# Kernel optimization log

Hardware: AMD Instinct MI355X
Metric: run time of the kernel (lower is better)

The kernel has to match this reference:

```python
import jax, jax.numpy as jnp
import numpy as np

N = 50000
E = 1600000
INDIM, HIDIM, OUTDIM = 256, 128, 64


def setup_inputs() -> dict:
    key = jax.random.key(0)
    ks = jax.random.split(key, 4)
    x = jax.random.normal(ks[0], (N, INDIM), dtype=jnp.float32)
    edge_index = jax.random.randint(ks[1], (2, E), 0, N, dtype=jnp.int32)
    W1 = jax.random.normal(ks[2], (INDIM, HIDIM), dtype=jnp.float32) / np.float32(np.sqrt(INDIM))
    b1 = jnp.zeros((HIDIM,), dtype=jnp.float32)
    W2 = jax.random.normal(ks[3], (HIDIM, OUTDIM), dtype=jnp.float32) / np.float32(np.sqrt(HIDIM))
    b2 = jnp.zeros((OUTDIM,), dtype=jnp.float32)
    return {"x": x, "edge_index": edge_index, "W1": W1, "b1": b1, "W2": W2, "b2": b2}


def _gcn_conv(x, row, col, norm, W, b):
    # PyG GCNConv: transform first, then normalized scatter-add aggregation, then bias
    h = x @ W                              # [N, out]
    msg = h[row] * norm[:, None]           # gather source features, scale by edge norm
    out = jax.ops.segment_sum(msg, col, num_segments=x.shape[0])  # scatter-add to dst
    return out + b


def reference(x, edge_index, W1, b1, W2, b2):
    n = x.shape[0]
    # add self loops (PyG default add_self_loops=True)
    loops = jnp.arange(n, dtype=edge_index.dtype)
    row = jnp.concatenate([edge_index[0], loops])  # source nodes
    col = jnp.concatenate([edge_index[1], loops])  # destination nodes
    # symmetric normalization: deg^{-1/2}[row] * deg^{-1/2}[col], deg over dst incl. self loops
    deg = jax.ops.segment_sum(jnp.ones_like(col, dtype=x.dtype), col, num_segments=n)
    dinv = jnp.where(deg > 0, jax.lax.rsqrt(jnp.maximum(deg, 1.0)), 0.0)
    norm = dinv[row] * dinv[col]
    h = jax.nn.relu(_gcn_conv(x, row, col, norm, W1, b1))
    return _gcn_conv(h, row, col, norm, W2, b2)
```

## Files before the change

### kernel.cpp

```cpp
#include <hip/hip_runtime.h>

#define NN 50000
#define NE 1600000
#define INDIM 256
#define HIDIM 128
#define OUTDIM 64

#define NRANGE 128
#define RSPAN 400
#define ACAP 16384
#define NBBLK 1563
#define NDEG 256

typedef unsigned int uint;
typedef unsigned long long ull;
typedef unsigned short ushort;
typedef __attribute__((ext_vector_type(8))) short bf16x8;
typedef __attribute__((ext_vector_type(4))) float f32x4;

__device__ __forceinline__ ushort f2bf(float f) {
    uint u = __float_as_uint(f);
    uint r = (u + 0x7FFFu + ((u >> 16) & 1u)) >> 16;
    return (ushort)r;
}
__device__ __forceinline__ uint pk2(float a, float b) {
    return (uint)f2bf(a) | ((uint)f2bf(b) << 16);
}
__device__ __forceinline__ float bf_lo(uint u) { return __uint_as_float(u << 16); }
__device__ __forceinline__ float bf_hi(uint u) { return __uint_as_float(u & 0xFFFF0000u); }

#define ACC8(u) do { \
    a0 += bf_lo((u).x); a1 += bf_hi((u).x); \
    a2 += bf_lo((u).y); a3 += bf_hi((u).y); \
    a4 += bf_lo((u).z); a5 += bf_hi((u).z); \
    a6 += bf_lo((u).w); a7 += bf_hi((u).w); \
} while (0)


__global__ void k_wt(const float* __restrict__ W1, const float* __restrict__ W2,
                     ushort* __restrict__ W1T, ushort* __restrict__ W2T) {
    int idx = blockIdx.x * 256 + threadIdx.x;
    if (idx < INDIM * HIDIM) {
        int k = idx / HIDIM, nn = idx % HIDIM;
        W1T[nn * INDIM + k] = f2bf(W1[idx]);
    } else {
        int j = idx - INDIM * HIDIM;
        if (j < HIDIM * OUTDIM) {
            int k = j / OUTDIM, nn = j % OUTDIM;
            W2T[nn * HIDIM + k] = f2bf(W2[j]);
        }
    }
}


__global__ void k_bcnt(const int* __restrict__ col, int* __restrict__ bcnt,
                       int* __restrict__ dhist) {
    __shared__ int bins[NRANGE];
    int tid = threadIdx.x;
    if (blockIdx.x == 0) dhist[tid] = 0;
    if (tid < NRANGE) bins[tid] = 0;
    __syncthreads();
    int base = blockIdx.x * 1024 + tid;
#pragma unroll
    for (int k = 0; k < 4; k++) {
        int i = base + k * 256;
        if (i < NE) atomicAdd(&bins[col[i] / RSPAN], 1);
    }
    __syncthreads();
    if (tid < NRANGE) bcnt[tid * NBBLK + blockIdx.x] = bins[tid];
}


__global__ void k_bscan(const int* __restrict__ bcnt, int* __restrict__ bbase,
                        int* __restrict__ rcur) {
    __shared__ int wsum[16];
    __shared__ int woff[16];
    int r = blockIdx.x;
    const int* src = bcnt + r * NBBLK;
    int* dst = bbase + r * NBBLK;
    int tid = threadIdx.x, lane = tid & 63, wid = tid >> 6;
    int seg = tid * 2;
    int l0 = (seg < NBBLK) ? src[seg] : 0;
    int l1 = (seg + 1 < NBBLK) ? src[seg + 1] : 0;
    int sum = l0 + l1;
    int incl = sum;
#pragma unroll
    for (int off = 1; off < 64; off <<= 1) {
        int t = __shfl_up(incl, off);
        if (lane >= off) incl += t;
    }
    if (lane == 63) wsum[wid] = incl;
    __syncthreads();
    if (wid == 0 && lane < 16) {
        int wv = wsum[lane];
        int wincl = wv;
#pragma unroll
        for (int off = 1; off < 16; off <<= 1) {
            int t = __shfl_up(wincl, off);
            if (lane >= off) wincl += t;
        }
        woff[lane] = wincl - wv;
    }
    __syncthreads();
    int run = incl - sum + woff[wid];
    if (seg < NBBLK) dst[seg] = run;
    if (seg + 1 < NBBLK) dst[seg + 1] = run + l0;
    if (tid == 1023) rcur[r] = run + sum;
}


__global__ void k_bscat(const int* __restrict__ row, const int* __restrict__ col,
                        const int* __restrict__ bbase, uint* __restrict__ staged) {
    __shared__ int cur[NRANGE];
    int tid = threadIdx.x;
    if (tid < NRANGE) cur[tid] = bbase[tid * NBBLK + blockIdx.x];
    __syncthreads();
    int base = blockIdx.x * 1024 + tid;
#pragma unroll
    for (int k = 0; k < 4; k++) {
        int i = base + k * 256;
        if (i < NE) {
            int d = col[i], s = row[i];
            int r = d / RSPAN;
            int off = atomicAdd(&cur[r], 1);
            staged[(size_t)r * ACAP + off] = ((uint)s << 10) | (uint)(d - r * RSPAN);
        }
    }
}


__global__ void k_sort(const uint* __restrict__ staged, const int* __restrict__ rcur,
                       int* __restrict__ row_ptr, float* __restrict__ dinv,
                       ushort* __restrict__ ssrc, int* __restrict__ dhist) {
    __shared__ int bins[RSPAN];
    __shared__ int wsum[16];
    __shared__ int woff[16];
    __shared__ int dh[NDEG];
    int r = blockIdx.x;
    int tid = threadIdx.x, lane = tid & 63, wid = tid >> 6;
    int lo = r * RSPAN;
    int count = rcur[r];
    int base = 0;
    for (int rr = 0; rr < r; rr++) base += rcur[rr];
    const uint* st = staged + (size_t)r * ACAP;

    if (tid < RSPAN) bins[tid] = 0;
    if (tid < NDEG) dh[tid] = 0;
    __syncthreads();

    for (int i = tid; i < count; i += 1024)
        atomicAdd(&bins[st[i] & 1023u], 1);
    __syncthreads();

    int v = (tid < RSPAN) ? bins[tid] : 0;
    int incl = v;
#pragma unroll
    for (int off = 1; off < 64; off <<= 1) {
        int t = __shfl_up(incl, off);
        if (lane >= off) incl += t;
    }
    if (lane == 63) wsum[wid] = incl;
    __syncthreads();
    if (wid == 0 && lane < 16) {
        int wv = wsum[lane];
        int wincl = wv;
#pragma unroll
        for (int off = 1; off < 16; off <<= 1) {
            int t = __shfl_up(wincl, off);
            if (lane >= off) wincl += t;
        }
        woff[lane] = wincl - wv;
    }
    __syncthreads();
    int excl = incl - v + woff[wid];
    int idx = lo + tid;
    if (tid < RSPAN && idx <= NN) {
        if (idx < NN) {
            row_ptr[idx] = base + excl;
            dinv[idx] = rsqrtf((float)(v + 1));
            atomicAdd(&dh[min(v, NDEG - 1)], 1);
        } else {
            row_ptr[NN] = base + excl;
        }
    }
    __syncthreads();
    if (tid < RSPAN) bins[tid] = base + excl;
    __syncthreads();
    if (tid < NDEG && dh[tid]) atomicAdd(&dhist[tid], dh[tid]);

    for (int i = tid; i < count; i += 1024) {
        uint rec = st[i];
        int pos = atomicAdd(&bins[rec & 1023u], 1);
        ssrc[pos] = (ushort)(rec >> 10);
    }
}


__global__ void k_dscan(const int* __restrict__ dhist, int* __restrict__ dcur) {
    int lane = threadIdx.x;
    int b = lane * 4;
    int v0 = dhist[b], v1 = dhist[b + 1], v2 = dhist[b + 2], v3 = dhist[b + 3];
    int s = v0 + v1 + v2 + v3;
    int incl = s;
#pragma unroll
    for (int off = 1; off < 64; off <<= 1) {
        int t = __shfl_up(incl, off);
        if (lane >= off) incl += t;
    }
    int excl = incl - s;
    dcur[b] = excl;
    dcur[b + 1] = excl + v0;
    dcur[b + 2] = excl + v0 + v1;
    dcur[b + 3] = excl + v0 + v1 + v2;
}


__global__ void k_dscat(const int* __restrict__ row_ptr, int* __restrict__ dcur,
                        int* __restrict__ perm) {
    __shared__ int h[NDEG];
    __shared__ int boff[NDEG];
    int tid = threadIdx.x;
    int d = blockIdx.x * 256 + tid;
    h[tid] = 0;
    __syncthreads();
    int bin = 0, myoff = 0;
    if (d < NN) {
        int deg = row_ptr[d + 1] - row_ptr[d];
        bin = min(deg, NDEG - 1);
        myoff = atomicAdd(&h[bin], 1);
    }
    __syncthreads();
    if (h[tid]) boff[tid] = atomicAdd(&dcur[tid], h[tid]);
    __syncthreads();
    if (d < NN) perm[boff[bin] + myoff] = d;
}


__global__ void k_gemm1(const float* __restrict__ A, const ushort* __restrict__ W1T,
                        const float* __restrict__ dinv, ushort* __restrict__ g1s, int n) {
    __shared__ ushort As[64 * 40];
    __shared__ ushort Bs[128 * 40];
    int tid = threadIdx.x;
    int w = tid >> 6, lane = tid & 63;
    int ln = lane & 15, quad = lane >> 4;
    int row0 = blockIdx.x * 64;
    int n0 = w * 32;

    f32x4 acc[4][2];
#pragma unroll
    for (int m = 0; m < 4; m++)
#pragma unroll
        for (int t = 0; t < 2; t++) acc[m][t] = (f32x4){0.f, 0.f, 0.f, 0.f};

    int ar = tid >> 2;
    int ac = (tid & 3) * 8;

    for (int k0 = 0; k0 < INDIM; k0 += 32) {
        {
            int gr = row0 + ar;
            uint4 u = make_uint4(0, 0, 0, 0);
            if (gr < n) {
                const float* p = A + (size_t)gr * INDIM + k0 + ac;
                float4 v0 = *(const float4*)p;
                float4 v1 = *(const float4*)(p + 4);
                u.x = pk2(v0.x, v0.y); u.y = pk2(v0.z, v0.w);
                u.z = pk2(v1.x, v1.y); u.w = pk2(v1.z, v1.w);
            }
            *(uint4*)(As + ar * 40 + ac) = u;
        }
#pragma unroll
        for (int it = 0; it < 2; it++) {
            int idx = tid + it * 256;
            int bn = idx >> 2, bc = (idx & 3) * 8;
            uint4 u = *(const uint4*)(W1T + (size_t)bn * INDIM + k0 + bc);
            *(uint4*)(Bs + bn * 40 + bc) = u;
        }
        __syncthreads();

        bf16x8 af[4], bf[2];
#pragma unroll
        for (int m = 0; m < 4; m++)
            af[m] = *(const bf16x8*)(As + (m * 16 + ln) * 40 + quad * 8);
#pragma unroll
        for (int t = 0; t < 2; t++)
            bf[t] = *(const bf16x8*)(Bs + (n0 + t * 16 + ln) * 40 + quad * 8);
#pragma unroll
        for (int m = 0; m < 4; m++)
#pragma unroll
            for (int t = 0; t < 2; t++)
                acc[m][t] = __builtin_amdgcn_mfma_f32_16x16x32_bf16(af[m], bf[t], acc[m][t], 0, 0, 0);
        __syncthreads();
    }

    int slice = w >> 1;
    int fbase = (w & 1) * 32;
#pragma unroll
    for (int m = 0; m < 4; m++) {
#pragma unroll
        for (int r = 0; r < 4; r++) {
            int gr = row0 + m * 16 + quad * 4 + r;
            if (gr < n) {
                float dv = dinv[gr];
#pragma unroll
                for (int t = 0; t < 2; t++) {
                    int cj = t * 16 + ln;
                    g1s[((size_t)slice * NN + gr) * 64 + fbase + cj] = f2bf(acc[m][t][r] * dv);
                }
            }
        }
    }
}


__global__ void k_agg1(const ushort* __restrict__ g1s, const float* __restrict__ dinv,
                       const int* __restrict__ row_ptr, const ushort* __restrict__ ssrc,
                       const int* __restrict__ perm, const float* __restrict__ b1,
                       ushort* __restrict__ hrb) {
    int slice = blockIdx.x & 1;
    int dbase = (blockIdx.x >> 1) * 32;
    int wid = threadIdx.x >> 6, lane = threadIdx.x & 63;
    int grp = lane >> 3, fl = lane & 7;
    int di = dbase + wid * 8 + grp;
    if (di >= NN) return;
    int d = perm[di];
    const ushort* gs = g1s + (size_t)slice * NN * 64 + fl * 8;
    float a0 = 0.f, a1 = 0.f, a2 = 0.f, a3 = 0.f;
    float a4 = 0.f, a5 = 0.f, a6 = 0.f, a7 = 0.f;
    int e0 = row_ptr[d], e1 = row_ptr[d + 1];
    if (e1 > e0) {
        int last = e1 - 1;
        int sB0 = ssrc[min(e0 + 0, last)];
        int sB1 = ssrc[min(e0 + 1, last)];
        int sB2 = ssrc[min(e0 + 2, last)];
        int sB3 = ssrc[min(e0 + 3, last)];
        uint4 uA0 = *(const uint4*)(gs + (size_t)sB0 * 64);
        uint4 uA1 = *(const uint4*)(gs + (size_t)sB1 * 64);
        uint4 uA2 = *(const uint4*)(gs + (size_t)sB2 * 64);
        uint4 uA3 = *(const uint4*)(gs + (size_t)sB3 * 64);
        sB0 = ssrc[min(e0 + 4, last)];
        sB1 = ssrc[min(e0 + 5, last)];
        sB2 = ssrc[min(e0 + 6, last)];
        sB3 = ssrc[min(e0 + 7, last)];
        for (int eb = e0; eb < e1; eb += 4) {
            int p0 = ssrc[min(eb + 8, last)];
            int p1 = ssrc[min(eb + 9, last)];
            int p2 = ssrc[min(eb + 10, last)];
            int p3 = ssrc[min(eb + 11, last)];
            uint4 v0 = *(const uint4*)(gs + (size_t)sB0 * 64);
            uint4 v1 = *(const uint4*)(gs + (size_t)sB1 * 64);
            uint4 v2 = *(const uint4*)(gs + (size_t)sB2 * 64);
            uint4 v3 = *(const uint4*)(gs + (size_t)sB3 * 64);
            uint4 z = make_uint4(0u, 0u, 0u, 0u);
            if (eb + 1 >= e1) uA1 = z;
            if (eb + 2 >= e1) uA2 = z;
            if (eb + 3 >= e1) uA3 = z;
            ACC8(uA0); ACC8(uA1); ACC8(uA2); ACC8(uA3);
            uA0 = v0; uA1 = v1; uA2 = v2; uA3 = v3;
            sB0 = p0; sB1 = p1; sB2 = p2; sB3 = p3;
        }
    }
    uint4 ud = *(const uint4*)(gs + (size_t)d * 64);
    ACC8(ud);
    float dv = dinv[d];
    const float* bp = b1 + slice * 64 + fl * 8;
    float4 bb0 = *(const float4*)bp;
    float4 bb1 = *(const float4*)(bp + 4);
    uint4 o;
    o.x = pk2(fmaxf(a0 * dv + bb0.x, 0.f), fmaxf(a1 * dv + bb0.y, 0.f));
    o.y = pk2(fmaxf(a2 * dv + bb0.z, 0.f), fmaxf(a3 * dv + bb0.w, 0.f));
    o.z = pk2(fmaxf(a4 * dv + bb1.x, 0.f), fmaxf(a5 * dv + bb1.y, 0.f));
    o.w = pk2(fmaxf(a6 * dv + bb1.z, 0.f), fmaxf(a7 * dv + bb1.w, 0.f));
    *(uint4*)(hrb + ((size_t)slice * NN + d) * 64 + fl * 8) = o;
}


__global__ void k_gemm2(const ushort* __restrict__ hrb, const ushort* __restrict__ W2T,
                        const float* __restrict__ dinv, ushort* __restrict__ g2s, int n) {
    __shared__ ushort As[64 * 40];
    __shared__ ushort Bs[64 * 40];
    int tid = threadIdx.x;
    int w = tid >> 6, lane = tid & 63;
    int ln = lane & 15, quad = lane >> 4;
    int row0 = blockIdx.x * 64;
    int n0 = w * 16;

    f32x4 acc[4];
#pragma unroll
    for (int m = 0; m < 4; m++) acc[m] = (f32x4){0.f, 0.f, 0.f, 0.f};

    int ar = tid >> 2;
    int ac = (tid & 3) * 8;

    for (int k0 = 0; k0 < HIDIM; k0 += 32) {
        {
            int gr = row0 + ar;
            uint4 u = make_uint4(0, 0, 0, 0);
            if (gr < n) u = *(const uint4*)(hrb + ((size_t)(k0 >> 6) * NN + gr) * 64 + (k0 & 63) + ac);
            *(uint4*)(As + ar * 40 + ac) = u;
        }
        {
            int bn = tid >> 2, bc = (tid & 3) * 8;
            uint4 u = *(const uint4*)(W2T + (size_t)bn * HIDIM + k0 + bc);
            *(uint4*)(Bs + bn * 40 + bc) = u;
        }
        __syncthreads();

        bf16x8 bf = *(const bf16x8*)(Bs + (n0 + ln) * 40 + quad * 8);
#pragma unroll
        for (int m = 0; m < 4; m++) {
            bf16x8 af = *(const bf16x8*)(As + (m * 16 + ln) * 40 + quad * 8);
            acc[m] = __builtin_amdgcn_mfma_f32_16x16x32_bf16(af, bf, acc[m], 0, 0, 0);
        }
        __syncthreads();
    }

    int col = n0 + ln;
#pragma unroll
    for (int m = 0; m < 4; m++) {
#pragma unroll
        for (int r = 0; r < 4; r++) {
            int gr = row0 + m * 16 + quad * 4 + r;
            if (gr < n) {
                g2s[(size_t)gr * 64 + col] = f2bf(acc[m][r] * dinv[gr]);
            }
        }
    }
}


__global__ void k_agg2(const ushort* __restrict__ g2s, const float* __restrict__ dinv,
                       const int* __restrict__ row_ptr, const ushort* __restrict__ ssrc,
                       const int* __restrict__ perm, const float* __restrict__ b2,
                       float* __restrict__ out) {
    int dbase = blockIdx.x * 32;
    int wid = threadIdx.x >> 6, lane = threadIdx.x & 63;
    int grp = lane >> 3, fl = lane & 7;
    int di = dbase + wid * 8 + grp;
    if (di >= NN) return;
    int d = perm[di];
    const ushort* gs = g2s + fl * 8;
    float a0 = 0.f, a1 = 0.f, a2 = 0.f, a3 = 0.f;
    float a4 = 0.f, a5 = 0.f, a6 = 0.f, a7 = 0.f;
    int e0 = row_ptr[d], e1 = row_ptr[d + 1];
    if (e1 > e0) {
        int last = e1 - 1;
        int sB0 = ssrc[min(e0 + 0, last)];
        int sB1 = ssrc[min(e0 + 1, last)];
        int sB2 = ssrc[min(e0 + 2, last)];
        int sB3 = ssrc[min(e0 + 3, last)];
        uint4 uA0 = *(const uint4*)(gs + (size_t)sB0 * 64);
        uint4 uA1 = *(const uint4*)(gs + (size_t)sB1 * 64);
        uint4 uA2 = *(const uint4*)(gs + (size_t)sB2 * 64);
        uint4 uA3 = *(const uint4*)(gs + (size_t)sB3 * 64);
        sB0 = ssrc[min(e0 + 4, last)];
        sB1 = ssrc[min(e0 + 5, last)];
        sB2 = ssrc[min(e0 + 6, last)];
        sB3 = ssrc[min(e0 + 7, last)];
        for (int eb = e0; eb < e1; eb += 4) {
            int p0 = ssrc[min(eb + 8, last)];
            int p1 = ssrc[min(eb + 9, last)];
            int p2 = ssrc[min(eb + 10, last)];
            int p3 = ssrc[min(eb + 11, last)];
            uint4 v0 = *(const uint4*)(gs + (size_t)sB0 * 64);
            uint4 v1 = *(const uint4*)(gs + (size_t)sB1 * 64);
            uint4 v2 = *(const uint4*)(gs + (size_t)sB2 * 64);
            uint4 v3 = *(const uint4*)(gs + (size_t)sB3 * 64);
            uint4 z = make_uint4(0u, 0u, 0u, 0u);
            if (eb + 1 >= e1) uA1 = z;
            if (eb + 2 >= e1) uA2 = z;
            if (eb + 3 >= e1) uA3 = z;
            ACC8(uA0); ACC8(uA1); ACC8(uA2); ACC8(uA3);
            uA0 = v0; uA1 = v1; uA2 = v2; uA3 = v3;
            sB0 = p0; sB1 = p1; sB2 = p2; sB3 = p3;
        }
    }
    uint4 ud = *(const uint4*)(gs + (size_t)d * 64);
    ACC8(ud);
    float dv = dinv[d];
    const float* bp = b2 + fl * 8;
    float4 bb0 = *(const float4*)bp;
    float4 bb1 = *(const float4*)(bp + 4);
    float4 r0, r1;
    r0.x = a0 * dv + bb0.x;
    r0.y = a1 * dv + bb0.y;
    r0.z = a2 * dv + bb0.z;
    r0.w = a3 * dv + bb0.w;
    r1.x = a4 * dv + bb1.x;
    r1.y = a5 * dv + bb1.y;
    r1.z = a6 * dv + bb1.z;
    r1.w = a7 * dv + bb1.w;
    float* op = out + (size_t)d * OUTDIM + fl * 8;
    *(float4*)op = r0;
    *(float4*)(op + 4) = r1;
}


extern "C" void kernel_launch(void* const* d_in, const int* in_sizes, int n_in,
                              void* d_out, int out_size, void* d_ws, size_t ws_size,
                              hipStream_t stream) {
    const float* x   = (const float*)d_in[0];
    const int*   ei  = (const int*)d_in[1];
    const float* W1  = (const float*)d_in[2];
    const float* b1  = (const float*)d_in[3];
    const float* W2  = (const float*)d_in[4];
    const float* b2  = (const float*)d_in[5];
    float* out = (float*)d_out;

    const int* row = ei;
    const int* col = ei + NE;

    size_t off = 0;
    auto alloc = [&](size_t bytes) {
        void* p = (char*)d_ws + off;
        off += (bytes + 255) & ~(size_t)255;
        return p;
    };
    float*  dinv     = (float*) alloc((size_t)NN * 4);
    int*    row_ptr  = (int*)   alloc((size_t)(NN + 1) * 4);
    int*    rcur     = (int*)   alloc(NRANGE * 4);
    int*    bcnt     = (int*)   alloc((size_t)NRANGE * NBBLK * 4);
    int*    bbase    = (int*)   alloc((size_t)NRANGE * NBBLK * 4);
    uint*   staged   = (uint*)  alloc((size_t)NRANGE * ACAP * 4);
    ushort* ssrc     = (ushort*)alloc((size_t)NE * 2);
    ushort* W1T      = (ushort*)alloc((size_t)INDIM * HIDIM * 2);
    ushort* W2T      = (ushort*)alloc((size_t)HIDIM * OUTDIM * 2);
    ushort* g1s      = (ushort*)alloc((size_t)NN * HIDIM * 2);
    ushort* hrb      = (ushort*)alloc((size_t)NN * HIDIM * 2);
    ushort* g2s      = (ushort*)alloc((size_t)NN * OUTDIM * 2);
    int*    dhist    = (int*)   alloc((size_t)NDEG * 4);
    int*    dcur     = (int*)   alloc((size_t)NDEG * 4);
    int*    perm     = (int*)   alloc((size_t)NN * 4);

    const int nb32 = (NN + 31) / 32;
    const int nb64 = (NN + 63) / 64;

    k_wt<<<(INDIM * HIDIM + HIDIM * OUTDIM + 255) / 256, 256, 0, stream>>>(W1, W2, W1T, W2T);

    k_bcnt<<<NBBLK, 256, 0, stream>>>(col, bcnt, dhist);
    k_bscan<<<NRANGE, 1024, 0, stream>>>(bcnt, bbase, rcur);
    k_bscat<<<NBBLK, 256, 0, stream>>>(row, col, bbase, staged);

    k_sort<<<NRANGE, 1024, 0, stream>>>(staged, rcur, row_ptr, dinv, ssrc, dhist);

    k_dscan<<<1, 64, 0, stream>>>(dhist, dcur);
    k_dscat<<<(NN + 255) / 256, 256, 0, stream>>>(row_ptr, dcur, perm);

    k_gemm1<<<nb64, 256, 0, stream>>>(x, W1T, dinv, g1s, NN);
    k_agg1<<<nb32 * 2, 256, 0, stream>>>(g1s, dinv, row_ptr, ssrc, perm, b1, hrb);
    k_gemm2<<<nb64, 256, 0, stream>>>(hrb, W2T, dinv, g2s, NN);
    k_agg2<<<nb32, 256, 0, stream>>>(g2s, dinv, row_ptr, ssrc, perm, b2, out);
}
```

Before: 231.4 us.

## Sort edges by source range within destination and unslice hidden feature layout

```diff
diff --git a/kernel.cpp b/kernel.cpp
--- a/kernel.cpp
+++ b/kernel.cpp
@@ -11,6 +11,9 @@
 #define ACAP 16384
 #define NBBLK 1563
 #define NDEG 256
+#define NSR 8
+#define SRD 6250
+#define SBINS (RSPAN * NSR)
 
 typedef unsigned int uint;
 typedef unsigned long long ull;
@@ -123,7 +126,8 @@
             int d = col[i], s = row[i];
             int r = d / RSPAN;
             int off = atomicAdd(&cur[r], 1);
-            staged[(size_t)r * ACAP + off] = ((uint)s << 10) | (uint)(d - r * RSPAN);
+            staged[(size_t)r * ACAP + off] =
+                ((uint)s << 12) | ((uint)(d - r * RSPAN) << 3) | (uint)(s / SRD);
         }
     }
 }
@@ -132,7 +136,7 @@
 __global__ void k_sort(const uint* __restrict__ staged, const int* __restrict__ rcur,
                        int* __restrict__ row_ptr, float* __restrict__ dinv,
                        ushort* __restrict__ ssrc, int* __restrict__ dhist) {
-    __shared__ int bins[RSPAN];
+    __shared__ int bins[SBINS];
     __shared__ int wsum[16];
     __shared__ int woff[16];
     __shared__ int dh[NDEG];
@@ -144,16 +148,21 @@
     for (int rr = 0; rr < r; rr++) base += rcur[rr];
     const uint* st = staged + (size_t)r * ACAP;
 
-    if (tid < RSPAN) bins[tid] = 0;
+    for (int b = tid; b < SBINS; b += 1024) bins[b] = 0;
     if (tid < NDEG) dh[tid] = 0;
     __syncthreads();
 
     for (int i = tid; i < count; i += 1024)
-        atomicAdd(&bins[st[i] & 1023u], 1);
-    __syncthreads();
-
-    int v = (tid < RSPAN) ? bins[tid] : 0;
-    int incl = v;
+        atomicAdd(&bins[st[i] & 0xFFFu], 1);
+    __syncthreads();
+
+    int seg = tid * 4;
+    int v0 = (seg + 0 < SBINS) ? bins[seg + 0] : 0;
+    int v1 = (seg + 1 < SBINS) ? bins[seg + 1] : 0;
+    int v2 = (seg + 2 < SBINS) ? bins[seg + 2] : 0;
+    int v3 = (seg + 3 < SBINS) ? bins[seg + 3] : 0;
+    int s4 = v0 + v1 + v2 + v3;
+    int incl = s4;
 #pragma unroll
     for (int off = 1; off < 64; off <<= 1) {
         int t = __shfl_up(incl, off);
@@ -172,26 +181,33 @@
         woff[lane] = wincl - wv;
     }
     __syncthreads();
-    int excl = incl - v + woff[wid];
+    int run = incl - s4 + woff[wid];
+    if (seg + 0 < SBINS) bins[seg + 0] = base + run;
+    if (seg + 1 < SBINS) bins[seg + 1] = base + run + v0;
+    if (seg + 2 < SBINS) bins[seg + 2] = base + run + v0 + v1;
+    if (seg + 3 < SBINS) bins[seg + 3] = base + run + v0 + v1 + v2;
+    __syncthreads();
+
     int idx = lo + tid;
     if (tid < RSPAN && idx <= NN) {
         if (idx < NN) {
-            row_ptr[idx] = base + excl;
-            dinv[idx] = rsqrtf((float)(v + 1));
-            atomicAdd(&dh[min(v, NDEG - 1)], 1);
+            int start = bins[tid * 8];
+            int end = (tid == RSPAN - 1) ? base + count : bins[(tid + 1) * 8];
+            int deg = end - start;
+            row_ptr[idx] = start;
+            dinv[idx] = rsqrtf((float)(deg + 1));
+            atomicAdd(&dh[min(deg, NDEG - 1)], 1);
         } else {
-            row_ptr[NN] = base + excl;
-        }
-    }
-    __syncthreads();
-    if (tid < RSPAN) bins[tid] = base + excl;
+            row_ptr[NN] = bins[0];
+        }
+    }
     __syncthreads();
     if (tid < NDEG && dh[tid]) atomicAdd(&dhist[tid], dh[tid]);
 
     for (int i = tid; i < count; i += 1024) {
         uint rec = st[i];
-        int pos = atomicAdd(&bins[rec & 1023u], 1);
-        ssrc[pos] = (ushort)(rec >> 10);
+        int pos = atomicAdd(&bins[rec & 0xFFFu], 1);
+        ssrc[pos] = (ushort)(rec >> 12);
     }
 }
 
@@ -292,8 +308,6 @@
         __syncthreads();
     }
 
-    int slice = w >> 1;
-    int fbase = (w & 1) * 32;
 #pragma unroll
     for (int m = 0; m < 4; m++) {
 #pragma unroll
@@ -304,7 +318,7 @@
 #pragma unroll
                 for (int t = 0; t < 2; t++) {
                     int cj = t * 16 + ln;
-                    g1s[((size_t)slice * NN + gr) * 64 + fbase + cj] = f2bf(acc[m][t][r] * dv);
+                    g1s[(size_t)gr * 128 + n0 + cj] = f2bf(acc[m][t][r] * dv);
                 }
             }
         }
@@ -316,14 +330,13 @@
                        const int* __restrict__ row_ptr, const ushort* __restrict__ ssrc,
                        const int* __restrict__ perm, const float* __restrict__ b1,
                        ushort* __restrict__ hrb) {
-    int slice = blockIdx.x & 1;
-    int dbase = (blockIdx.x >> 1) * 32;
+    int dbase = blockIdx.x * 16;
     int wid = threadIdx.x >> 6, lane = threadIdx.x & 63;
-    int grp = lane >> 3, fl = lane & 7;
-    int di = dbase + wid * 8 + grp;
+    int grp = lane >> 4, fl = lane & 15;
+    int di = dbase + wid * 4 + grp;
     if (di >= NN) return;
     int d = perm[di];
-    const ushort* gs = g1s + (size_t)slice * NN * 64 + fl * 8;
+    const ushort* gs = g1s + fl * 8;
     float a0 = 0.f, a1 = 0.f, a2 = 0.f, a3 = 0.f;
     float a4 = 0.f, a5 = 0.f, a6 = 0.f, a7 = 0.f;
     int e0 = row_ptr[d], e1 = row_ptr[d + 1];
@@ -333,10 +346,10 @@
         int sB1 = ssrc[min(e0 + 1, last)];
         int sB2 = ssrc[min(e0 + 2, last)];
         int sB3 = ssrc[min(e0 + 3, last)];
-        uint4 uA0 = *(const uint4*)(gs + (size_t)sB0 * 64);
-        uint4 uA1 = *(const uint4*)(gs + (size_t)sB1 * 64);
-        uint4 uA2 = *(const uint4*)(gs + (size_t)sB2 * 64);
-        uint4 uA3 = *(const uint4*)(gs + (size_t)sB3 * 64);
+        uint4 uA0 = *(const uint4*)(gs + (size_t)sB0 * 128);
+        uint4 uA1 = *(const uint4*)(gs + (size_t)sB1 * 128);
+        uint4 uA2 = *(const uint4*)(gs + (size_t)sB2 * 128);
+        uint4 uA3 = *(const uint4*)(gs + (size_t)sB3 * 128);
         sB0 = ssrc[min(e0 + 4, last)];
         sB1 = ssrc[min(e0 + 5, last)];
         sB2 = ssrc[min(e0 + 6, last)];
@@ -346,10 +359,10 @@
             int p1 = ssrc[min(eb + 9, last)];
             int p2 = ssrc[min(eb + 10, last)];
             int p3 = ssrc[min(eb + 11, last)];
-            uint4 v0 = *(const uint4*)(gs + (size_t)sB0 * 64);
-            uint4 v1 = *(const uint4*)(gs + (size_t)sB1 * 64);
-            uint4 v2 = *(const uint4*)(gs + (size_t)sB2 * 64);
-            uint4 v3 = *(const uint4*)(gs + (size_t)sB3 * 64);
+            uint4 v0 = *(const uint4*)(gs + (size_t)sB0 * 128);
+            uint4 v1 = *(const uint4*)(gs + (size_t)sB1 * 128);
+            uint4 v2 = *(const uint4*)(gs + (size_t)sB2 * 128);
+            uint4 v3 = *(const uint4*)(gs + (size_t)sB3 * 128);
             uint4 z = make_uint4(0u, 0u, 0u, 0u);
             if (eb + 1 >= e1) uA1 = z;
             if (eb + 2 >= e1) uA2 = z;
@@ -359,10 +372,10 @@
             sB0 = p0; sB1 = p1; sB2 = p2; sB3 = p3;
         }
     }
-    uint4 ud = *(const uint4*)(gs + (size_t)d * 64);
+    uint4 ud = *(const uint4*)(gs + (size_t)d * 128);
     ACC8(ud);
     float dv = dinv[d];
-    const float* bp = b1 + slice * 64 + fl * 8;
+    const float* bp = b1 + fl * 8;
     float4 bb0 = *(const float4*)bp;
     float4 bb1 = *(const float4*)(bp + 4);
     uint4 o;
@@ -370,7 +383,7 @@
     o.y = pk2(fmaxf(a2 * dv + bb0.z, 0.f), fmaxf(a3 * dv + bb0.w, 0.f));
     o.z = pk2(fmaxf(a4 * dv + bb1.x, 0.f), fmaxf(a5 * dv + bb1.y, 0.f));
     o.w = pk2(fmaxf(a6 * dv + bb1.z, 0.f), fmaxf(a7 * dv + bb1.w, 0.f));
-    *(uint4*)(hrb + ((size_t)slice * NN + d) * 64 + fl * 8) = o;
+    *(uint4*)(hrb + (size_t)d * 128 + fl * 8) = o;
 }
 
 
@@ -395,7 +408,7 @@
         {
             int gr = row0 + ar;
             uint4 u = make_uint4(0, 0, 0, 0);
-            if (gr < n) u = *(const uint4*)(hrb + ((size_t)(k0 >> 6) * NN + gr) * 64 + (k0 & 63) + ac);
+            if (gr < n) u = *(const uint4*)(hrb + (size_t)gr * 128 + k0 + ac);
             *(uint4*)(As + ar * 40 + ac) = u;
         }
         {
@@ -531,6 +544,7 @@
     int*    dcur     = (int*)   alloc((size_t)NDEG * 4);
     int*    perm     = (int*)   alloc((size_t)NN * 4);
 
+    const int nb16 = (NN + 15) / 16;
     const int nb32 = (NN + 31) / 32;
     const int nb64 = (NN + 63) / 64;
 
@@ -546,7 +560,7 @@
     k_dscat<<<(NN + 255) / 256, 256, 0, stream>>>(row_ptr, dcur, perm);
 
     k_gemm1<<<nb64, 256, 0, stream>>>(x, W1T, dinv, g1s, NN);
-    k_agg1<<<nb32 * 2, 256, 0, stream>>>(g1s, dinv, row_ptr, ssrc, perm, b1, hrb);
+    k_agg1<<<nb16, 256, 0, stream>>>(g1s, dinv, row_ptr, ssrc, perm, b1, hrb);
     k_gemm2<<<nb64, 256, 0, stream>>>(hrb, W2T, dinv, g2s, NN);
     k_agg2<<<nb32, 256, 0, stream>>>(g2s, dinv, row_ptr, ssrc, perm, b2, out);
 }
```

After: 232.7 us. No clear change (+0.6%).

## Build degree-permuted CSR so aggregation reads edges and node data contiguously

Applied to the files above, without the earlier changes.

```diff
diff --git a/kernel.cpp b/kernel.cpp
--- a/kernel.cpp
+++ b/kernel.cpp
@@ -196,43 +196,71 @@
 }
 
 
-__global__ void k_dscan(const int* __restrict__ dhist, int* __restrict__ dcur) {
+__global__ void k_dscan(const int* __restrict__ dhist, int* __restrict__ dstart,
+                        int* __restrict__ dcur, int* __restrict__ ebase) {
     int lane = threadIdx.x;
     int b = lane * 4;
     int v0 = dhist[b], v1 = dhist[b + 1], v2 = dhist[b + 2], v3 = dhist[b + 3];
+    int w0 = v0 * b, w1 = v1 * (b + 1), w2 = v2 * (b + 2), w3 = v3 * (b + 3);
     int s = v0 + v1 + v2 + v3;
-    int incl = s;
+    int sw = w0 + w1 + w2 + w3;
+    int incl = s, inclw = sw;
 #pragma unroll
     for (int off = 1; off < 64; off <<= 1) {
         int t = __shfl_up(incl, off);
-        if (lane >= off) incl += t;
-    }
-    int excl = incl - s;
-    dcur[b] = excl;
-    dcur[b + 1] = excl + v0;
-    dcur[b + 2] = excl + v0 + v1;
-    dcur[b + 3] = excl + v0 + v1 + v2;
-}
-
-
-__global__ void k_dscat(const int* __restrict__ row_ptr, int* __restrict__ dcur,
-                        int* __restrict__ perm) {
+        int t2 = __shfl_up(inclw, off);
+        if (lane >= off) { incl += t; inclw += t2; }
+    }
+    int excl = incl - s, exclw = inclw - sw;
+    dstart[b] = excl;            dcur[b] = excl;            ebase[b] = exclw;
+    dstart[b + 1] = excl + v0;   dcur[b + 1] = excl + v0;   ebase[b + 1] = exclw + w0;
+    dstart[b + 2] = excl + v0 + v1; dcur[b + 2] = excl + v0 + v1; ebase[b + 2] = exclw + w0 + w1;
+    dstart[b + 3] = excl + v0 + v1 + v2; dcur[b + 3] = excl + v0 + v1 + v2; ebase[b + 3] = exclw + w0 + w1 + w2;
+}
+
+
+__global__ void k_dscat(const int* __restrict__ row_ptr, const float* __restrict__ dinv,
+                        const int* __restrict__ dstart, int* __restrict__ dcur,
+                        const int* __restrict__ ebase, int* __restrict__ perm,
+                        int* __restrict__ row_ptr_p, float* __restrict__ dinv_p) {
     __shared__ int h[NDEG];
     __shared__ int boff[NDEG];
     int tid = threadIdx.x;
     int d = blockIdx.x * 256 + tid;
     h[tid] = 0;
     __syncthreads();
-    int bin = 0, myoff = 0;
+    int bin = 0, myoff = 0, deg = 0;
     if (d < NN) {
-        int deg = row_ptr[d + 1] - row_ptr[d];
+        deg = row_ptr[d + 1] - row_ptr[d];
         bin = min(deg, NDEG - 1);
         myoff = atomicAdd(&h[bin], 1);
     }
     __syncthreads();
     if (h[tid]) boff[tid] = atomicAdd(&dcur[tid], h[tid]);
     __syncthreads();
-    if (d < NN) perm[boff[bin] + myoff] = d;
+    if (d < NN) {
+        int di = boff[bin] + myoff;
+        perm[di] = d;
+        int grank = di - dstart[bin];
+        row_ptr_p[di] = ebase[bin] + grank * deg;
+        dinv_p[di] = dinv[d];
+    }
+    if (d == 0) row_ptr_p[NN] = NE;
+}
+
+
+__global__ void k_csrperm(const int* __restrict__ perm, const int* __restrict__ row_ptr,
+                          const int* __restrict__ row_ptr_p, const ushort* __restrict__ ssrc,
+                          ushort* __restrict__ ssrc_p) {
+    int g = blockIdx.x * 256 + threadIdx.x;
+    int di = g >> 2, j = g & 3;
+    if (di >= NN) return;
+    int d = perm[di];
+    int e0p = row_ptr_p[di];
+    int deg = row_ptr_p[di + 1] - e0p;
+    int e0 = row_ptr[d];
+    for (int k = j; k < deg; k += 4)
+        ssrc_p[e0p + k] = ssrc[e0 + k];
 }
 
 
@@ -312,8 +340,8 @@
 }
 
 
-__global__ void k_agg1(const ushort* __restrict__ g1s, const float* __restrict__ dinv,
-                       const int* __restrict__ row_ptr, const ushort* __restrict__ ssrc,
+__global__ void k_agg1(const ushort* __restrict__ g1s, const float* __restrict__ dinv_p,
+                       const int* __restrict__ row_ptr_p, const ushort* __restrict__ ssrc_p,
                        const int* __restrict__ perm, const float* __restrict__ b1,
                        ushort* __restrict__ hrb) {
     int slice = blockIdx.x & 1;
@@ -326,26 +354,26 @@
     const ushort* gs = g1s + (size_t)slice * NN * 64 + fl * 8;
     float a0 = 0.f, a1 = 0.f, a2 = 0.f, a3 = 0.f;
     float a4 = 0.f, a5 = 0.f, a6 = 0.f, a7 = 0.f;
-    int e0 = row_ptr[d], e1 = row_ptr[d + 1];
+    int e0 = row_ptr_p[di], e1 = row_ptr_p[di + 1];
     if (e1 > e0) {
         int last = e1 - 1;
-        int sB0 = ssrc[min(e0 + 0, last)];
-        int sB1 = ssrc[min(e0 + 1, last)];
-        int sB2 = ssrc[min(e0 + 2, last)];
-        int sB3 = ssrc[min(e0 + 3, last)];
+        int sB0 = ssrc_p[min(e0 + 0, last)];
+        int sB1 = ssrc_p[min(e0 + 1, last)];
+        int sB2 = ssrc_p[min(e0 + 2, last)];
+        int sB3 = ssrc_p[min(e0 + 3, last)];
         uint4 uA0 = *(const uint4*)(gs + (size_t)sB0 * 64);
         uint4 uA1 = *(const uint4*)(gs + (size_t)sB1 * 64);
         uint4 uA2 = *(const uint4*)(gs + (size_t)sB2 * 64);
         uint4 uA3 = *(const uint4*)(gs + (size_t)sB3 * 64);
-        sB0 = ssrc[min(e0 + 4, last)];
-        sB1 = ssrc[min(e0 + 5, last)];
-        sB2 = ssrc[min(e0 + 6, last)];
-        sB3 = ssrc[min(e0 + 7, last)];
+        sB0 = ssrc_p[min(e0 + 4, last)];
+        sB1 = ssrc_p[min(e0 + 5, last)];
+        sB2 = ssrc_p[min(e0 + 6, last)];
+        sB3 = ssrc_p[min(e0 + 7, last)];
         for (int eb = e0; eb < e1; eb += 4) {
-            int p0 = ssrc[min(eb + 8, last)];
-            int p1 = ssrc[min(eb + 9, last)];
-            int p2 = ssrc[min(eb + 10, last)];
-            int p3 = ssrc[min(eb + 11, last)];
+            int p0 = ssrc_p[min(eb + 8, last)];
+            int p1 = ssrc_p[min(eb + 9, last)];
+            int p2 = ssrc_p[min(eb + 10, last)];
+            int p3 = ssrc_p[min(eb + 11, last)];
             uint4 v0 = *(const uint4*)(gs + (size_t)sB0 * 64);
             uint4 v1 = *(const uint4*)(gs + (size_t)sB1 * 64);
             uint4 v2 = *(const uint4*)(gs + (size_t)sB2 * 64);
@@ -361,7 +389,7 @@
     }
     uint4 ud = *(const uint4*)(gs + (size_t)d * 64);
     ACC8(ud);
-    float dv = dinv[d];
+    float dv = dinv_p[di];
     const float* bp = b1 + slice * 64 + fl * 8;
     float4 bb0 = *(const float4*)bp;
     float4 bb1 = *(const float4*)(bp + 4);
@@ -370,12 +398,13 @@
     o.y = pk2(fmaxf(a2 * dv + bb0.z, 0.f), fmaxf(a3 * dv + bb0.w, 0.f));
     o.z = pk2(fmaxf(a4 * dv + bb1.x, 0.f), fmaxf(a5 * dv + bb1.y, 0.f));
     o.w = pk2(fmaxf(a6 * dv + bb1.z, 0.f), fmaxf(a7 * dv + bb1.w, 0.f));
-    *(uint4*)(hrb + ((size_t)slice * NN + d) * 64 + fl * 8) = o;
+    *(uint4*)(hrb + ((size_t)slice * NN + di) * 64 + fl * 8) = o;
 }
 
 
 __global__ void k_gemm2(const ushort* __restrict__ hrb, const ushort* __restrict__ W2T,
-                        const float* __restrict__ dinv, ushort* __restrict__ g2s, int n) {
+                        const float* __restrict__ dinv_p, const int* __restrict__ perm,
+                        ushort* __restrict__ g2s, int n) {
     __shared__ ushort As[64 * 40];
     __shared__ ushort Bs[64 * 40];
     int tid = threadIdx.x;
@@ -421,15 +450,16 @@
         for (int r = 0; r < 4; r++) {
             int gr = row0 + m * 16 + quad * 4 + r;
             if (gr < n) {
-                g2s[(size_t)gr * 64 + col] = f2bf(acc[m][r] * dinv[gr]);
+                int gd = perm[gr];
+                g2s[(size_t)gd * 64 + col] = f2bf(acc[m][r] * dinv_p[gr]);
             }
         }
     }
 }
 
 
-__global__ void k_agg2(const ushort* __restrict__ g2s, const float* __restrict__ dinv,
-                       const int* __restrict__ row_ptr, const ushort* __restrict__ ssrc,
+__global__ void k_agg2(const ushort* __restrict__ g2s, const float* __restrict__ dinv_p,
+                       const int* __restrict__ row_ptr_p, const ushort* __restrict__ ssrc_p,
                        const int* __restrict__ perm, const float* __restrict__ b2,
                        float* __restrict__ out) {
     int dbase = blockIdx.x * 32;
@@ -441,26 +471,26 @@
     const ushort* gs = g2s + fl * 8;
     float a0 = 0.f, a1 = 0.f, a2 = 0.f, a3 = 0.f;
     float a4 = 0.f, a5 = 0.f, a6 = 0.f, a7 = 0.f;
-    int e0 = row_ptr[d], e1 = row_ptr[d + 1];
+    int e0 = row_ptr_p[di], e1 = row_ptr_p[di + 1];
     if (e1 > e0) {
         int last = e1 - 1;
-        int sB0 = ssrc[min(e0 + 0, last)];
-        int sB1 = ssrc[min(e0 + 1, last)];
-        int sB2 = ssrc[min(e0 + 2, last)];
-        int sB3 = ssrc[min(e0 + 3, last)];
+        int sB0 = ssrc_p[min(e0 + 0, last)];
+        int sB1 = ssrc_p[min(e0 + 1, last)];
+        int sB2 = ssrc_p[min(e0 + 2, last)];
+        int sB3 = ssrc_p[min(e0 + 3, last)];
         uint4 uA0 = *(const uint4*)(gs + (size_t)sB0 * 64);
         uint4 uA1 = *(const uint4*)(gs + (size_t)sB1 * 64);
         uint4 uA2 = *(const uint4*)(gs + (size_t)sB2 * 64);
         uint4 uA3 = *(const uint4*)(gs + (size_t)sB3 * 64);
-        sB0 = ssrc[min(e0 + 4, last)];
-        sB1 = ssrc[min(e0 + 5, last)];
-        sB2 = ssrc[min(e0 + 6, last)];
-        sB3 = ssrc[min(e0 + 7, last)];
+        sB0 = ssrc_p[min(e0 + 4, last)];
+        sB1 = ssrc_p[min(e0 + 5, last)];
+        sB2 = ssrc_p[min(e0 + 6, last)];
+        sB3 = ssrc_p[min(e0 + 7, last)];
         for (int eb = e0; eb < e1; eb += 4) {
-            int p0 = ssrc[min(eb + 8, last)];
-            int p1 = ssrc[min(eb + 9, last)];
-            int p2 = ssrc[min(eb + 10, last)];
-            int p3 = ssrc[min(eb + 11, last)];
+            int p0 = ssrc_p[min(eb + 8, last)];
+            int p1 = ssrc_p[min(eb + 9, last)];
+            int p2 = ssrc_p[min(eb + 10, last)];
+            int p3 = ssrc_p[min(eb + 11, last)];
             uint4 v0 = *(const uint4*)(gs + (size_t)sB0 * 64);
             uint4 v1 = *(const uint4*)(gs + (size_t)sB1 * 64);
             uint4 v2 = *(const uint4*)(gs + (size_t)sB2 * 64);
@@ -476,7 +506,7 @@
     }
     uint4 ud = *(const uint4*)(gs + (size_t)d * 64);
     ACC8(ud);
-    float dv = dinv[d];
+    float dv = dinv_p[di];
     const float* bp = b2 + fl * 8;
     float4 bb0 = *(const float4*)bp;
     float4 bb1 = *(const float4*)(bp + 4);
@@ -522,14 +552,19 @@
     int*    bbase    = (int*)   alloc((size_t)NRANGE * NBBLK * 4);
     uint*   staged   = (uint*)  alloc((size_t)NRANGE * ACAP * 4);
     ushort* ssrc     = (ushort*)alloc((size_t)NE * 2);
+    ushort* ssrc_p   = (ushort*)alloc((size_t)NE * 2);
     ushort* W1T      = (ushort*)alloc((size_t)INDIM * HIDIM * 2);
     ushort* W2T      = (ushort*)alloc((size_t)HIDIM * OUTDIM * 2);
     ushort* g1s      = (ushort*)alloc((size_t)NN * HIDIM * 2);
     ushort* hrb      = (ushort*)alloc((size_t)NN * HIDIM * 2);
     ushort* g2s      = (ushort*)alloc((size_t)NN * OUTDIM * 2);
     int*    dhist    = (int*)   alloc((size_t)NDEG * 4);
+    int*    dstart   = (int*)   alloc((size_t)NDEG * 4);
     int*    dcur     = (int*)   alloc((size_t)NDEG * 4);
+    int*    ebase    = (int*)   alloc((size_t)NDEG * 4);
     int*    perm     = (int*)   alloc((size_t)NN * 4);
+    int*    row_ptr_p= (int*)   alloc((size_t)(NN + 1) * 4);
+    float*  dinv_p   = (float*) alloc((size_t)NN * 4);
 
     const int nb32 = (NN + 31) / 32;
     const int nb64 = (NN + 63) / 64;
@@ -542,11 +577,13 @@
 
     k_sort<<<NRANGE, 1024, 0, stream>>>(staged, rcur, row_ptr, dinv, ssrc, dhist);
 
-    k_dscan<<<1, 64, 0, stream>>>(dhist, dcur);
-    k_dscat<<<(NN + 255) / 256, 256, 0, stream>>>(row_ptr, dcur, perm);
+    k_dscan<<<1, 64, 0, stream>>>(dhist, dstart, dcur, ebase);
+    k_dscat<<<(NN + 255) / 256, 256, 0, stream>>>(row_ptr, dinv, dstart, dcur, ebase,
+                                                  perm, row_ptr_p, dinv_p);
+    k_csrperm<<<(NN * 4 + 255) / 256, 256, 0, stream>>>(perm, row_ptr, row_ptr_p, ssrc, ssrc_p);
 
     k_gemm1<<<nb64, 256, 0, stream>>>(x, W1T, dinv, g1s, NN);
-    k_agg1<<<nb32 * 2, 256, 0, stream>>>(g1s, dinv, row_ptr, ssrc, perm, b1, hrb);
-    k_gemm2<<<nb64, 256, 0, stream>>>(hrb, W2T, dinv, g2s, NN);
-    k_agg2<<<nb32, 256, 0, stream>>>(g2s, dinv, row_ptr, ssrc, perm, b2, out);
-}
+    k_agg1<<<nb32 * 2, 256, 0, stream>>>(g1s, dinv_p, row_ptr_p, ssrc_p, perm, b1, hrb);
+    k_gemm2<<<nb64, 256, 0, stream>>>(hrb, W2T, dinv_p, perm, g2s, NN);
+    k_agg2<<<nb32, 256, 0, stream>>>(g2s, dinv_p, row_ptr_p, ssrc_p, perm, b2, out);
+}
```

Measured after the change: 228.6 us. No clear change (-1.2%).
